# Optimization experiments

Measured on AMD Instinct MI355X. Metric: run time of the kernel, lower is better.

## Reference

```python
import jax, jax.numpy as jnp
import numpy as np

N_FFT = 512
HOP = 128
WIN = 512
BATCH = 32
N_SAMPLES = 480000


def make_forward_basis():
    n_freq = N_FFT // 2 + 1  # 257
    # periodic hann window (torch.hann_window default periodic=True)
    n = np.arange(WIN, dtype=np.float32)
    window = 0.5 * (1.0 - np.cos(2.0 * np.pi * n / WIN))
    freqs = np.linspace(0.0, N_FFT // 2, n_freq, dtype=np.float32)  # [n_freq]
    t = np.arange(WIN, dtype=np.float32)
    phase = 2.0 * np.pi * freqs[:, None] * t[None, :] / N_FFT
    real = np.cos(phase) * window[None, :]
    imag = -np.sin(phase) * window[None, :]
    basis = np.concatenate([real, imag], axis=0)[:, None, :]
    return jnp.asarray(basis, dtype=jnp.float32)


def setup_inputs() -> dict:
    key = jax.random.key(0)
    x = jax.random.normal(key, (BATCH, N_SAMPLES), dtype=jnp.float32)
    return {"x": x, "forward_basis": make_forward_basis()}


def reference(x, forward_basis):
    # x: [B, T] -> [B, 1, T]
    x = x[:, None, :]
    pad = N_FFT // 2
    x_padded = jnp.pad(x, ((0, 0), (0, 0), (pad, pad)), mode="reflect")
    # single conv over concatenated real+imag basis: [B, 2*n_freq, n_frames]
    spec = jax.lax.conv_general_dilated(
        x_padded, forward_basis,
        window_strides=(HOP,), padding="VALID",
        dimension_numbers=("NCH", "OIH", "NCH"))
    n_freq = N_FFT // 2 + 1
    real_spec = spec[:, :n_freq, :]
    imag_spec = spec[:, n_freq:, :]
    return jnp.sqrt(real_spec ** 2 + imag_spec ** 2)
```

## Files before the change

kernel.cpp:

```cpp
#include <hip/hip_runtime.h>

#define NFREQ   257
#define NFRAMES 3751
#define NS      480000
#define HOP     128
#define WIN     512

#define NB      32
#define BN      128
#define NFT     30
#define STEPS   32
#define XWPITCH 272
#define XW_B    35632
#define WNYQ_B  2048
#define XGROUPS 2096

typedef __attribute__((ext_vector_type(8))) short short8;
typedef __attribute__((ext_vector_type(4))) float f32x4;

__device__ __forceinline__ short f2bf(float f) {
    __bf16 b = (__bf16)f;
    return __builtin_bit_cast(short, b);
}
__device__ __forceinline__ float bf2f(short s) {
    unsigned int u = ((unsigned int)(unsigned short)s) << 16;
    return __builtin_bit_cast(float, u);
}

__global__ __launch_bounds__(256)
void prep_basis9(const float* __restrict__ basis,
                 short* __restrict__ abL, short* __restrict__ wnyqG) {
    int g = blockIdx.x * 256 + threadIdx.x;
    if (g < 32768) {
        int ob   = g * 16;
        int step = ob >> 14;
        int w    = (ob >> 12) & 3;
        int pl   = (ob >> 11) & 1;
        int m    = (ob >> 10) & 1;
        int lane = (ob >> 4) & 63;
        int l15  = lane & 15;
        int lgrp = lane >> 4;
        int fr   = (step >> 4) * 128 + w * 32 + m * 16 + l15;
        int k0   = (step & 15) * 32 + lgrp * 8;
        const float4* p = reinterpret_cast<const float4*>(
            basis + ((size_t)(pl * NFREQ + fr)) * WIN + k0);
        float4 a0 = p[0], a1 = p[1];
        short8 v;
        v[0]=f2bf(a0.x); v[1]=f2bf(a0.y); v[2]=f2bf(a0.z); v[3]=f2bf(a0.w);
        v[4]=f2bf(a1.x); v[5]=f2bf(a1.y); v[6]=f2bf(a1.z); v[7]=f2bf(a1.w);
        *reinterpret_cast<short8*>(reinterpret_cast<char*>(abL) + ob) = v;
    } else if (g < 32832) {
        int j = g - 32768;
        const float4* p = reinterpret_cast<const float4*>(basis + (size_t)256 * WIN + j * 8);
        float4 a0 = p[0], a1 = p[1];
        short8 v;
        v[0]=f2bf(a0.x); v[1]=f2bf(a0.y); v[2]=f2bf(a0.z); v[3]=f2bf(a0.w);
        v[4]=f2bf(a1.x); v[5]=f2bf(a1.y); v[6]=f2bf(a1.z); v[7]=f2bf(a1.w);
        *reinterpret_cast<short8*>(wnyqG + j * 8) = v;
    }
}

__global__ __launch_bounds__(256, 2)
void stft_mfma_kernel(const float* __restrict__ x,
                      const short* __restrict__ abL,
                      const short* __restrict__ wnyqG,
                      float* __restrict__ out)
{
    __shared__ __align__(16) char smem[XW_B + WNYQ_B];
    char* const xw   = smem;
    float* const wny = reinterpret_cast<float*>(smem + XW_B);

    const int tid  = threadIdx.x;
    const int wave = tid >> 6;
    const int lane = tid & 63;
    const int lgrp = lane >> 4;
    const int l15  = lane & 15;

    const int logical = (blockIdx.x & 7) * 120 + (blockIdx.x >> 3);
    const int ft = logical % NFT;
    const int b  = logical / NFT;
    const int t0 = ft * BN;

    const char* const aS = (const char*)abL + (wave << 12) + lane * 16;

    {
        short a0 = wnyqG[tid * 2], a1 = wnyqG[tid * 2 + 1];
        wny[tid * 2]     = bf2f(a0);
        wny[tid * 2 + 1] = bf2f(a1);
    }

    {
        const float* __restrict__ xb = x + (size_t)b * NS;
        const int sbase = t0 * 128 - 256;
        #pragma unroll
        for (int i = 0; i < 9; ++i) {
            int g = tid + i * 256;
            if (g < XGROUPS) {
                int ix = sbase + g * 8;
                short8 v;
                if (ix >= 0 && ix + 8 <= NS) {
                    const float4* p = reinterpret_cast<const float4*>(xb + ix);
                    float4 a0 = p[0], a1 = p[1];
                    v[0]=f2bf(a0.x); v[1]=f2bf(a0.y); v[2]=f2bf(a0.z); v[3]=f2bf(a0.w);
                    v[4]=f2bf(a1.x); v[5]=f2bf(a1.y); v[6]=f2bf(a1.z); v[7]=f2bf(a1.w);
                } else {
                    #pragma unroll
                    for (int q = 0; q < 8; ++q) {
                        int idx = ix + q;
                        if (idx < 0) idx = -idx;
                        if (idx >= NS + 256) { v[q] = 0; continue; }
                        if (idx >= NS) idx = 2 * NS - 2 - idx;
                        v[q] = f2bf(xb[idx]);
                    }
                }
                *reinterpret_cast<short8*>(xw + (g >> 4) * XWPITCH + (g & 15) * 16) = v;
            }
        }
    }
    __syncthreads();

    f32x4 accR[2][8], accI[2][8];
    #pragma unroll
    for (int m = 0; m < 2; ++m)
        #pragma unroll
        for (int n = 0; n < 8; ++n) {
            accR[m][n] = f32x4{0.f,0.f,0.f,0.f};
            accI[m][n] = f32x4{0.f,0.f,0.f,0.f};
        }

    const int nfl = wave * 32 + (lane & 31);
    const int nh  = lane >> 5;
    const int nyqXbase = (nfl + 2 * nh) * XWPITCH;
    const float* const nyqW = wny + nh * 256;
    float nacc = 0.f;

    short8 R0[2], I0[2], R1[2], I1[2];

    #define ALOAD(RS, IS, s)                                                        \
    {                                                                               \
        const char* p_ = aS + (size_t)(s) * 16384;                                  \
        (RS)[0] = *reinterpret_cast<const short8*>(p_);                             \
        (RS)[1] = *reinterpret_cast<const short8*>(p_ + 1024);                      \
        (IS)[0] = *reinterpret_cast<const short8*>(p_ + 2048);                      \
        (IS)[1] = *reinterpret_cast<const short8*>(p_ + 3072);                      \
    }

    #define COMPUTE(s, R, I)                                                        \
    {                                                                               \
        short8 xv[8];                                                               \
        {                                                                           \
            int r8 = ((s) & 15) * 64 + lgrp * 16;                                   \
            int T  = r8 + ((r8 >> 8) << 4);                                         \
            const char* xwl = xw + l15 * XWPITCH + T;                               \
            _Pragma("unroll")                                                       \
            for (int nt = 0; nt < 8; ++nt)                                          \
                xv[nt] = *reinterpret_cast<const short8*>(xwl + nt * (16 * XWPITCH)); \
        }                                                                           \
        {                 \
            short8 nx = *reinterpret_cast<const short8*>(                           \
                xw + nyqXbase + ((s) >> 4) * XWPITCH + ((s) & 15) * 16);            \
            const float* wrow = nyqW + (s) * 8;                                     \
            _Pragma("unroll")                                                       \
            for (int q = 0; q < 8; ++q)                                             \
                nacc = fmaf(bf2f(nx[q]), wrow[q], nacc);                            \
        }                                                                           \
        __builtin_amdgcn_s_setprio(1);                                              \
        _Pragma("unroll")                                                           \
        for (int m = 0; m < 2; ++m)                                                 \
            _Pragma("unroll")                                                       \
            for (int nt = 0; nt < 8; ++nt) {                                        \
                accR[m][nt] = __builtin_amdgcn_mfma_f32_16x16x32_bf16(              \
                    (R)[m], xv[nt], accR[m][nt], 0, 0, 0);                          \
                accI[m][nt] = __builtin_amdgcn_mfma_f32_16x16x32_bf16(              \
                    (I)[m], xv[nt], accI[m][nt], 0, 0, 0);                          \
            }                                                                       \
        __builtin_amdgcn_s_setprio(0);                                              \
    }

    #define EPILOGUE(fp)                                                            \
    {                                                                               \
        float* ob = out + (size_t)b * NFREQ * NFRAMES;                              \
        const int fb = (fp) * 128 + wave * 32 + lgrp * 4;                           \
        const int tb = t0 + l15;                                                    \
        _Pragma("unroll")                                                           \
        for (int m = 0; m < 2; ++m)                                                 \
            _Pragma("unroll")                                                       \
            for (int nt = 0; nt < 8; ++nt) {                                        \
                int t = tb + nt * 16;                                               \
                if (t < NFRAMES) {                                                  \
                    _Pragma("unroll")                                               \
                    for (int r = 0; r < 4; ++r) {                                   \
                        int f = fb + m * 16 + r;                                    \
                        float vr = accR[m][nt][r], vi = accI[m][nt][r];             \
                        ob[(size_t)f * NFRAMES + t] =                               \
                            __builtin_amdgcn_sqrtf(vr * vr + vi * vi);              \
                    }                                                               \
                }                                                                   \
                accR[m][nt] = f32x4{0.f,0.f,0.f,0.f};                               \
                accI[m][nt] = f32x4{0.f,0.f,0.f,0.f};                               \
            }                                                                       \
    }

    ALOAD(R0, I0, 0);

    #pragma unroll 1
    for (int s = 0; s < STEPS; s += 2) {
        ALOAD(R1, I1, s + 1);
        COMPUTE(s, R0, I0);
        if (s + 2 < STEPS) ALOAD(R0, I0, s + 2);
        COMPUTE(s + 1, R1, I1);
        if ((s & 15) == 14) EPILOGUE(s >> 4);
    }

    {
        nacc += __shfl_xor(nacc, 32);
        int t = t0 + nfl;
        if (nh == 0 && t < NFRAMES)
            out[((size_t)b * NFREQ + 256) * NFRAMES + t] = fabsf(nacc);
    }
}

extern "C" void kernel_launch(void* const* d_in, const int* in_sizes, int n_in,
                              void* d_out, int out_size, void* d_ws, size_t ws_size,
                              hipStream_t stream) {
    const float* x     = (const float*)d_in[0];
    const float* basis = (const float*)d_in[1];
    float* out = (float*)d_out;

    short* abL   = (short*)d_ws;
    short* wnyqG = abL + 262144;

    prep_basis9<<<dim3(129), 256, 0, stream>>>(basis, abL, wnyqG);
    stft_mfma_kernel<<<dim3(NFT * NB), 256, 0, stream>>>(x, abL, wnyqG, out);
}
```

Baseline: 73.33 us.

## Switch STFT GEMM from 16x16x32 to 32x32x16 bf16 MFMA tiles

Replaces the 16x16x32 MFMA tiling with 32x32x16 MFMA instructions, reorganizing the basis prep layout, the LDS fragment loads, the accumulators and the epilogue index mapping to match. Larger MFMA tiles carry more work per instruction and give better operand reuse per LDS read, which aims to cut instruction-issue and LDS traffic overhead. Accumulator register count stays the same. The epilogue store pattern changes (frequency rows strided by 8), which may affect write coalescing.

```diff
diff --git a/kernel.cpp b/kernel.cpp
--- a/kernel.cpp
+++ b/kernel.cpp
@@ -15,8 +15,8 @@
 #define WNYQ_B  2048
 #define XGROUPS 2096
 
-typedef __attribute__((ext_vector_type(8))) short short8;
-typedef __attribute__((ext_vector_type(4))) float f32x4;
+typedef __attribute__((ext_vector_type(8)))  short short8;
+typedef __attribute__((ext_vector_type(16))) float f32x16;
 
 __device__ __forceinline__ short f2bf(float f) {
     __bf16 b = (__bf16)f;
@@ -28,20 +28,18 @@
 }
 
 __global__ __launch_bounds__(256)
-void prep_basis9(const float* __restrict__ basis,
-                 short* __restrict__ abL, short* __restrict__ wnyqG) {
+void prep_basis10(const float* __restrict__ basis,
+                  short* __restrict__ abL, short* __restrict__ wnyqG) {
     int g = blockIdx.x * 256 + threadIdx.x;
     if (g < 32768) {
         int ob   = g * 16;
         int step = ob >> 14;
         int w    = (ob >> 12) & 3;
         int pl   = (ob >> 11) & 1;
-        int m    = (ob >> 10) & 1;
+        int kh   = (ob >> 10) & 1;
         int lane = (ob >> 4) & 63;
-        int l15  = lane & 15;
-        int lgrp = lane >> 4;
-        int fr   = (step >> 4) * 128 + w * 32 + m * 16 + l15;
-        int k0   = (step & 15) * 32 + lgrp * 8;
+        int fr   = (step >> 4) * 128 + w * 32 + (lane & 31);
+        int k0   = (step & 15) * 32 + kh * 16 + (lane >> 5) * 8;
         const float4* p = reinterpret_cast<const float4*>(
             basis + ((size_t)(pl * NFREQ + fr)) * WIN + k0);
         float4 a0 = p[0], a1 = p[1];
@@ -73,8 +71,8 @@
     const int tid  = threadIdx.x;
     const int wave = tid >> 6;
     const int lane = tid & 63;
-    const int lgrp = lane >> 4;
-    const int l15  = lane & 15;
+    const int l31  = lane & 31;
+    const int lhi  = lane >> 5;
 
     const int logical = (blockIdx.x & 7) * 120 + (blockIdx.x >> 3);
     const int ft = logical % NFT;
@@ -119,17 +117,14 @@
     }
     __syncthreads();
 
-    f32x4 accR[2][8], accI[2][8];
+    f32x16 accR[4], accI[4];
     #pragma unroll
-    for (int m = 0; m < 2; ++m)
+    for (int tt = 0; tt < 4; ++tt)
         #pragma unroll
-        for (int n = 0; n < 8; ++n) {
-            accR[m][n] = f32x4{0.f,0.f,0.f,0.f};
-            accI[m][n] = f32x4{0.f,0.f,0.f,0.f};
-        }
-
-    const int nfl = wave * 32 + (lane & 31);
-    const int nh  = lane >> 5;
+        for (int e = 0; e < 16; ++e) { accR[tt][e] = 0.f; accI[tt][e] = 0.f; }
+
+    const int nfl = wave * 32 + l31;
+    const int nh  = lhi;
     const int nyqXbase = (nfl + 2 * nh) * XWPITCH;
     const float* const nyqW = wny + nh * 256;
     float nacc = 0.f;
@@ -149,12 +144,15 @@
     {                                                                               \
         short8 xv[8];                                                               \
         {                                                                           \
-            int r8 = ((s) & 15) * 64 + lgrp * 16;                                   \
-            int T  = r8 + ((r8 >> 8) << 4);                                         \
-            const char* xwl = xw + l15 * XWPITCH + T;                               \
             _Pragma("unroll")                                                       \
-            for (int nt = 0; nt < 8; ++nt)                                          \
-                xv[nt] = *reinterpret_cast<const short8*>(xwl + nt * (16 * XWPITCH)); \
+            for (int tt = 0; tt < 4; ++tt)                                          \
+                _Pragma("unroll")                                                   \
+                for (int kh = 0; kh < 2; ++kh) {                                    \
+                    int r8 = ((s) & 15) * 64 + kh * 32 + lhi * 16;                  \
+                    int T  = r8 + ((r8 >> 8) << 4);                                 \
+                    xv[tt * 2 + kh] = *reinterpret_cast<const short8*>(             \
+                        xw + (tt * 32 + l31) * XWPITCH + T);                        \
+                }                                                                   \
         }                                                                           \
         {                 \
             short8 nx = *reinterpret_cast<const short8*>(                           \
@@ -166,39 +164,38 @@
         }                                                                           \
         __builtin_amdgcn_s_setprio(1);                                              \
         _Pragma("unroll")                                                           \
-        for (int m = 0; m < 2; ++m)                                                 \
-            _Pragma("unroll")                                                       \
-            for (int nt = 0; nt < 8; ++nt) {                                        \
-                accR[m][nt] = __builtin_amdgcn_mfma_f32_16x16x32_bf16(              \
-                    (R)[m], xv[nt], accR[m][nt], 0, 0, 0);                          \
-                accI[m][nt] = __builtin_amdgcn_mfma_f32_16x16x32_bf16(              \
-                    (I)[m], xv[nt], accI[m][nt], 0, 0, 0);                          \
-            }                                                                       \
+        for (int tt = 0; tt < 4; ++tt) {                                            \
+            accR[tt] = __builtin_amdgcn_mfma_f32_32x32x16_bf16(                     \
+                (R)[0], xv[tt * 2 + 0], accR[tt], 0, 0, 0);                         \
+            accR[tt] = __builtin_amdgcn_mfma_f32_32x32x16_bf16(                     \
+                (R)[1], xv[tt * 2 + 1], accR[tt], 0, 0, 0);                         \
+            accI[tt] = __builtin_amdgcn_mfma_f32_32x32x16_bf16(                     \
+                (I)[0], xv[tt * 2 + 0], accI[tt], 0, 0, 0);                         \
+            accI[tt] = __builtin_amdgcn_mfma_f32_32x32x16_bf16(                     \
+                (I)[1], xv[tt * 2 + 1], accI[tt], 0, 0, 0);                         \
+        }                                                                           \
         __builtin_amdgcn_s_setprio(0);                                              \
     }
 
     #define EPILOGUE(fp)                                                            \
     {                                                                               \
         float* ob = out + (size_t)b * NFREQ * NFRAMES;                              \
-        const int fb = (fp) * 128 + wave * 32 + lgrp * 4;                           \
-        const int tb = t0 + l15;                                                    \
+        const int fb = (fp) * 128 + wave * 32 + 4 * lhi;                            \
         _Pragma("unroll")                                                           \
-        for (int m = 0; m < 2; ++m)                                                 \
+        for (int tt = 0; tt < 4; ++tt) {                                            \
+            int t = t0 + tt * 32 + l31;                                             \
+            if (t < NFRAMES) {                                                      \
+                _Pragma("unroll")                                                   \
+                for (int r = 0; r < 16; ++r) {                                      \
+                    int f = fb + (r & 3) + 8 * (r >> 2);                            \
+                    float vr = accR[tt][r], vi = accI[tt][r];                       \
+                    ob[(size_t)f * NFRAMES + t] =                                   \
+                        __builtin_amdgcn_sqrtf(vr * vr + vi * vi);                  \
+                }                                                                   \
+            }                                                                       \
             _Pragma("unroll")                                                       \
-            for (int nt = 0; nt < 8; ++nt) {                                        \
-                int t = tb + nt * 16;                                               \
-                if (t < NFRAMES) {                                                  \
-                    _Pragma("unroll")                                               \
-                    for (int r = 0; r < 4; ++r) {                                   \
-                        int f = fb + m * 16 + r;                                    \
-                        float vr = accR[m][nt][r], vi = accI[m][nt][r];             \
-                        ob[(size_t)f * NFRAMES + t] =                               \
-                            __builtin_amdgcn_sqrtf(vr * vr + vi * vi);              \
-                    }                                                               \
-                }                                                                   \
-                accR[m][nt] = f32x4{0.f,0.f,0.f,0.f};                               \
-                accI[m][nt] = f32x4{0.f,0.f,0.f,0.f};                               \
-            }                                                                       \
+            for (int e = 0; e < 16; ++e) { accR[tt][e] = 0.f; accI[tt][e] = 0.f; }  \
+        }                                                                           \
     }
 
     ALOAD(R0, I0, 0);
@@ -230,6 +227,6 @@
     short* abL   = (short*)d_ws;
     short* wnyqG = abL + 262144;
 
-    prep_basis9<<<dim3(129), 256, 0, stream>>>(basis, abL, wnyqG);
+    prep_basis10<<<dim3(129), 256, 0, stream>>>(basis, abL, wnyqG);
     stft_mfma_kernel<<<dim3(NFT * NB), 256, 0, stream>>>(x, abL, wnyqG, out);
 }
```

Measured after the change: 84.92 us. 15.8% more time.
